# Performance work log

Measured on AMD Instinct MI355X. Metric: run time of the kernel, lower is better.

The kernel has to match this reference:

```python
import jax, jax.numpy as jnp
import numpy as np

B, R, C, A, K = 32, 13, 13, 5, 20
CELL = K + 5                      # 4 coords + objectness + 20 classes
N = R * C * A                     # 845 boxes per image
THRESH = 0.5
NMS_TH = 0.4
BIAS_VALS = [1.3221, 1.73145, 3.19275, 4.00944, 5.05587,
             8.09892, 9.47112, 4.84053, 11.2364, 10.0071]


def setup_inputs() -> dict:
    key = jax.random.key(0)
    x = jax.random.normal(key, (B, R, C, A * CELL), dtype=jnp.float32)
    bias = jnp.array(BIAS_VALS, dtype=jnp.float32)  # anchor priors (w,h interleaved)
    return {"x": x, "bias": bias}


def _nms_keep(iou, scores):
    """Greedy per-class NMS. iou: [B,N,N]; scores: [B,K,N] (already thresholded).
    Returns bool keep mask [B,K,N]. Decisions are non-differentiable, so inputs
    are stop_gradient'ed by the caller."""
    Bn = scores.shape[0]
    valid = scores > THRESH
    order = jnp.argsort(-scores, axis=-1)          # descending score order [B,K,N]
    rank = jnp.argsort(order, axis=-1)             # inverse permutation   [B,K,N]
    barange = jnp.arange(Bn)[:, None]

    def body(i, suppressed):
        idx = order[:, :, i]                                              # [B,K]
        sup_i = jnp.take_along_axis(suppressed, idx[:, :, None], -1)[..., 0]
        val_i = jnp.take_along_axis(valid, idx[:, :, None], -1)[..., 0]
        alive = val_i & ~sup_i                                            # [B,K]
        row = iou[barange, idx]                                           # [B,K,N]
        return suppressed | (alive[..., None] & (row > NMS_TH) & (rank > i))

    suppressed = jax.lax.fori_loop(0, N, body, jnp.zeros((Bn, K, N), bool))
    return valid & ~suppressed


def reference(x, bias):
    Bn, R_, C_, _ = x.shape
    t = x.reshape(Bn, R_, C_, A, CELL)
    gx = jnp.arange(C_, dtype=x.dtype)
    gy = jnp.arange(R_, dtype=x.dtype)
    # box decode (matches source: hNorm=rows used for width, wNorm=cols for height)
    bx = (jax.nn.sigmoid(t[..., 0]) + gx[None, None, :, None]) / C_
    by = (jax.nn.sigmoid(t[..., 1]) + gy[None, :, None, None]) / R_
    bw = jnp.exp(t[..., 2]) * bias[0::2] / R_
    bh = jnp.exp(t[..., 3]) * bias[1::2] / C_
    obj = jax.nn.sigmoid(t[..., 4])
    cls = jax.nn.softmax(t[..., 5:], axis=-1)
    prob = obj[..., None] * cls
    prob = jnp.where(prob > THRESH, prob, 0.0)

    # flatten to box index layout (y*cols + x)*anchors + a, same as source
    flat = lambda a: a.reshape(Bn, N)
    bx, by, bw, bh, obj = map(flat, (bx, by, bw, bh, obj))
    prob = prob.reshape(Bn, N, K)

    # corner-form boxes for IoU (source uses x - w/2, y - h/2, w, h)
    x1 = bx - bw * 0.5
    y1 = by - bh * 0.5
    x2 = x1 + bw
    y2 = y1 + bh
    iw = jnp.maximum(0.0, jnp.minimum(x2[:, :, None], x2[:, None, :]) -
                          jnp.maximum(x1[:, :, None], x1[:, None, :]))
    ih = jnp.maximum(0.0, jnp.minimum(y2[:, :, None], y2[:, None, :]) -
                          jnp.maximum(y1[:, :, None], y1[:, None, :]))
    inter = iw * ih
    area = bw * bh
    union = area[:, :, None] + area[:, None, :] - inter
    iou = inter / jnp.maximum(union, 1e-9)                       # [B,N,N]

    scores = prob.transpose(0, 2, 1)                             # [B,K,N]
    keep = _nms_keep(jax.lax.stop_gradient(iou),
                     jax.lax.stop_gradient(scores))
    out_prob = jnp.where(keep, scores, 0.0).transpose(0, 2, 1)   # [B,N,K]

    out = jnp.concatenate([bx[..., None], by[..., None], bw[..., None],
                           bh[..., None], obj[..., None], out_prob], axis=-1)
    return out  # [B, N, CELL]
```

## Files before the change

### kernel.cpp

```cpp
#include <hip/hip_runtime.h>
#include <math.h>

#define BN 32
#define RR 13
#define CC 13
#define AA 5
#define KK 20
#define CELLSZ 25
#define NN (RR * CC * AA)
#define NBK (BN * KK)
#define THRESH 0.5f
#define NMS_TH 0.4f

#define CAND_OFF 4096
#define REC 8
#define CAP NN

__device__ __forceinline__ float sigmoidf_(float x) {
    return 1.0f / (1.0f + expf(-x));
}

__global__ __launch_bounds__(256) void decode_kernel(
        const float* __restrict__ x,
        const float* __restrict__ bias,
        float* __restrict__ out,
        int* __restrict__ cnt,
        float* __restrict__ cand) {
    int idx = blockIdx.x * 256 + threadIdx.x;
    if (idx >= BN * NN) return;
    int b   = idx / NN;
    int n   = idx % NN;
    int r   = n / (CC * AA);
    int rem = n % (CC * AA);
    int c   = rem / AA;
    int a   = rem % AA;

    const float* t = x + (size_t)idx * CELLSZ;

    float bx  = (sigmoidf_(t[0]) + (float)c) / (float)CC;
    float by  = (sigmoidf_(t[1]) + (float)r) / (float)RR;
    float bw  = expf(t[2]) * bias[2 * a]     / (float)RR;
    float bh  = expf(t[3]) * bias[2 * a + 1] / (float)CC;
    float obj = sigmoidf_(t[4]);

    float l[KK];
    float m = t[5];
#pragma unroll
    for (int k = 0; k < KK; ++k) { l[k] = t[5 + k]; m = fmaxf(m, l[k]); }
    float s = 0.0f;
#pragma unroll
    for (int k = 0; k < KK; ++k) { l[k] = expf(l[k] - m); s += l[k]; }

    float* o = out + (size_t)idx * CELLSZ;
    o[0] = bx; o[1] = by; o[2] = bw; o[3] = bh; o[4] = obj;
#pragma unroll
    for (int k = 0; k < KK; ++k) o[5 + k] = 0.0f;

#pragma unroll
    for (int k = 0; k < KK; ++k) {
        float p = obj * (l[k] / s);
        if (p > THRESH) {
            int bk   = b * KK + k;
            int slot = atomicAdd(&cnt[bk], 1);
            float* rec = cand + ((size_t)bk * CAP + slot) * REC;
            float x1 = bx - bw * 0.5f;
            float y1 = by - bh * 0.5f;
            rec[0] = __int_as_float(n);
            rec[1] = p;
            rec[2] = x1;
            rec[3] = y1;
            rec[4] = x1 + bw;
            rec[5] = y1 + bh;
            rec[6] = bw * bh;
        }
    }
}

__global__ __launch_bounds__(64) void nms_kernel(
        const int* __restrict__ cnt,
        const float* __restrict__ cand,
        float* __restrict__ out) {
    int bk = blockIdx.x;
    int m  = cnt[bk];
    if (m <= 0) return;
    int b    = bk / KK;
    int k    = bk % KK;
    int lane = threadIdx.x;
    const float* list = cand + (size_t)bk * CAP * REC;

    if (m == 1) {
        if (lane == 0) {
            int n = __float_as_int(list[0]);
            out[((size_t)b * NN + n) * CELLSZ + 5 + k] = list[1];
        }
        return;
    }

    int T = (m + 63) >> 6;
    unsigned alive = 0;
    for (int tt = 0; tt < T; ++tt) {
        int j = lane + (tt << 6);
        if (j < m) alive |= 1u << tt;
    }

    while (true) {
        float bs = -1.0f;
        int   bn = 0x7fffffff;
        int   bg = -1;
        for (int tt = 0; tt < T; ++tt) {
            if ((alive >> tt) & 1u) {
                int j = lane + (tt << 6);
                float sc = list[j * REC + 1];
                int   nn = __float_as_int(list[j * REC]);
                if (sc > bs || (sc == bs && nn < bn)) { bs = sc; bn = nn; bg = j; }
            }
        }
#pragma unroll
        for (int off = 32; off > 0; off >>= 1) {
            float os = __shfl_xor(bs, off);
            int   on = __shfl_xor(bn, off);
            int   og = __shfl_xor(bg, off);
            if (os > bs || (os == bs && on < bn)) { bs = os; bn = on; bg = og; }
        }
        if (bg < 0) break;

        float X1 = list[bg * REC + 2];
        float Y1 = list[bg * REC + 3];
        float X2 = list[bg * REC + 4];
        float Y2 = list[bg * REC + 5];
        float AR = list[bg * REC + 6];

        if ((bg & 63) == lane) {
            out[((size_t)b * NN + bn) * CELLSZ + 5 + k] = bs;
            alive &= ~(1u << (bg >> 6));
        }

        for (int tt = 0; tt < T; ++tt) {
            int j = lane + (tt << 6);
            if (((alive >> tt) & 1u) && j != bg) {
                float iw = fmaxf(0.0f, fminf(X2, list[j * REC + 4]) - fmaxf(X1, list[j * REC + 2]));
                float ih = fmaxf(0.0f, fminf(Y2, list[j * REC + 5]) - fmaxf(Y1, list[j * REC + 3]));
                float inter = iw * ih;
                float uni   = AR + list[j * REC + 6] - inter;
                float iou   = inter / fmaxf(uni, 1e-9f);
                if (iou > NMS_TH) alive &= ~(1u << tt);
            }
        }
    }
}

extern "C" void kernel_launch(void* const* d_in, const int* in_sizes, int n_in,
                              void* d_out, int out_size, void* d_ws, size_t ws_size,
                              hipStream_t stream) {
    const float* x    = (const float*)d_in[0];
    const float* bias = (const float*)d_in[1];
    float* out = (float*)d_out;

    int*   cnt  = (int*)d_ws;
    float* cand = (float*)((char*)d_ws + CAND_OFF);

    hipMemsetAsync(cnt, 0, NBK * sizeof(int), stream);
    decode_kernel<<<(BN * NN + 255) / 256, 256, 0, stream>>>(x, bias, out, cnt, cand);
    nms_kernel<<<NBK, 64, 0, stream>>>(cnt, cand, out);
}
```

Baseline: 62.59 us.

## Fuse decode and per-class NMS into one block-per-image kernel using shared memory

Replaces the memset, decode kernel and per-(batch,class) NMS kernel with a single kernel that runs one 1024-thread block per image. The block stages the image in LDS, decodes there, and keeps candidate boxes in shared arrays; NMS then runs per class, one wave per class. It uses the fact that with threshold 0.5 only the argmax class can pass (two softmax probabilities cannot both exceed 0.5), so each box makes at most one candidate. This removes two launches, the global atomics and the global candidate round trip. In exchange only 32 blocks run, which leaves most CUs idle, and the shared-memory footprint is large.

```diff
diff --git a/kernel.cpp b/kernel.cpp
--- a/kernel.cpp
+++ b/kernel.cpp
@@ -8,145 +8,126 @@
 #define KK 20
 #define CELLSZ 25
 #define NN (RR * CC * AA)
-#define NBK (BN * KK)
+#define TOT (NN * CELLSZ)
 #define THRESH 0.5f
 #define NMS_TH 0.4f
+#define NT 1024
 
-#define CAND_OFF 4096
-#define REC 8
-#define CAP NN
-
-__device__ __forceinline__ float sigmoidf_(float x) {
-    return 1.0f / (1.0f + expf(-x));
-}
-
-__global__ __launch_bounds__(256) void decode_kernel(
+__global__ __launch_bounds__(NT) void region_kernel(
         const float* __restrict__ x,
         const float* __restrict__ bias,
-        float* __restrict__ out,
-        int* __restrict__ cnt,
-        float* __restrict__ cand) {
-    int idx = blockIdx.x * 256 + threadIdx.x;
-    if (idx >= BN * NN) return;
-    int b   = idx / NN;
-    int n   = idx % NN;
-    int r   = n / (CC * AA);
-    int rem = n % (CC * AA);
-    int c   = rem / AA;
-    int a   = rem % AA;
+        float* __restrict__ out)
+{
+    __shared__ float sraw[TOT];
+    __shared__ int   pcnt;
+    __shared__ int   kcnt[KK];
+    __shared__ int   ctag[NN], cidx[NN];
+    __shared__ float csc[NN], px1[NN], py1[NN], px2[NN], py2[NN], par[NN];
 
-    const float* t = x + (size_t)idx * CELLSZ;
+    const int b   = blockIdx.x;
+    const int tid = threadIdx.x;
+    const float* xb = x   + (size_t)b * TOT;
+    float*       ob = out + (size_t)b * TOT;
 
-    float bx  = (sigmoidf_(t[0]) + (float)c) / (float)CC;
-    float by  = (sigmoidf_(t[1]) + (float)r) / (float)RR;
-    float bw  = expf(t[2]) * bias[2 * a]     / (float)RR;
-    float bh  = expf(t[3]) * bias[2 * a + 1] / (float)CC;
-    float obj = sigmoidf_(t[4]);
+    if (tid == 0) pcnt = 0;
+    if (tid < KK) kcnt[tid] = 0;
 
-    float l[KK];
-    float m = t[5];
+    for (int i = tid; i < TOT; i += NT) sraw[i] = xb[i];
+    __syncthreads();
+
+    if (tid < NN) {
+        const int n  = tid;
+        int r   = n / (CC * AA);
+        int rem = n - r * (CC * AA);
+        int c   = rem / AA;
+        int a   = rem - c * AA;
+        float* t = sraw + n * CELLSZ;
+
+        float bx  = (1.f / (1.f + expf(-t[0])) + (float)c) / (float)CC;
+        float by  = (1.f / (1.f + expf(-t[1])) + (float)r) / (float)RR;
+        float bw  = expf(t[2]) * bias[2 * a]     / (float)RR;
+        float bh  = expf(t[3]) * bias[2 * a + 1] / (float)CC;
+        float obj = 1.f / (1.f + expf(-t[4]));
+
+        float l[KK];
+        float m = t[5];
 #pragma unroll
-    for (int k = 0; k < KK; ++k) { l[k] = t[5 + k]; m = fmaxf(m, l[k]); }
-    float s = 0.0f;
+        for (int k = 0; k < KK; ++k) { l[k] = t[5 + k]; m = fmaxf(m, l[k]); }
+        float s = 0.f;
 #pragma unroll
-    for (int k = 0; k < KK; ++k) { l[k] = expf(l[k] - m); s += l[k]; }
+        for (int k = 0; k < KK; ++k) s += expf(l[k] - m);
+        int km = 0;
+#pragma unroll
+        for (int k = 1; k < KK; ++k) if (l[k] > l[km]) km = k;
 
-    float* o = out + (size_t)idx * CELLSZ;
-    o[0] = bx; o[1] = by; o[2] = bw; o[3] = bh; o[4] = obj;
+        float p = obj * (1.0f / s);
+
+        t[0] = bx; t[1] = by; t[2] = bw; t[3] = bh; t[4] = obj;
 #pragma unroll
-    for (int k = 0; k < KK; ++k) o[5 + k] = 0.0f;
+        for (int k = 0; k < KK; ++k) t[5 + k] = 0.f;
 
-#pragma unroll
-    for (int k = 0; k < KK; ++k) {
-        float p = obj * (l[k] / s);
         if (p > THRESH) {
-            int bk   = b * KK + k;
-            int slot = atomicAdd(&cnt[bk], 1);
-            float* rec = cand + ((size_t)bk * CAP + slot) * REC;
-            float x1 = bx - bw * 0.5f;
-            float y1 = by - bh * 0.5f;
-            rec[0] = __int_as_float(n);
-            rec[1] = p;
-            rec[2] = x1;
-            rec[3] = y1;
-            rec[4] = x1 + bw;
-            rec[5] = y1 + bh;
-            rec[6] = bw * bh;
+            int slot = atomicAdd(&pcnt, 1);
+            atomicAdd(&kcnt[km], 1);
+            ctag[slot] = km; cidx[slot] = n; csc[slot] = p;
+            float x1 = bx - bw * 0.5f, y1 = by - bh * 0.5f;
+            px1[slot] = x1; py1[slot] = y1;
+            px2[slot] = x1 + bw; py2[slot] = y1 + bh;
+            par[slot] = bw * bh;
         }
     }
-}
+    __syncthreads();
 
-__global__ __launch_bounds__(64) void nms_kernel(
-        const int* __restrict__ cnt,
-        const float* __restrict__ cand,
-        float* __restrict__ out) {
-    int bk = blockIdx.x;
-    int m  = cnt[bk];
-    if (m <= 0) return;
-    int b    = bk / KK;
-    int k    = bk % KK;
-    int lane = threadIdx.x;
-    const float* list = cand + (size_t)bk * CAP * REC;
+    const int mtot = pcnt;
+    const int wave = tid >> 6;
+    const int lane = tid & 63;
+    const int T    = (mtot + 63) >> 6;
 
-    if (m == 1) {
-        if (lane == 0) {
-            int n = __float_as_int(list[0]);
-            out[((size_t)b * NN + n) * CELLSZ + 5 + k] = list[1];
-        }
-        return;
-    }
-
-    int T = (m + 63) >> 6;
-    unsigned alive = 0;
-    for (int tt = 0; tt < T; ++tt) {
-        int j = lane + (tt << 6);
-        if (j < m) alive |= 1u << tt;
-    }
-
-    while (true) {
-        float bs = -1.0f;
-        int   bn = 0x7fffffff;
-        int   bg = -1;
-        for (int tt = 0; tt < T; ++tt) {
-            if ((alive >> tt) & 1u) {
-                int j = lane + (tt << 6);
-                float sc = list[j * REC + 1];
-                int   nn = __float_as_int(list[j * REC]);
-                if (sc > bs || (sc == bs && nn < bn)) { bs = sc; bn = nn; bg = j; }
-            }
-        }
-#pragma unroll
-        for (int off = 32; off > 0; off >>= 1) {
-            float os = __shfl_xor(bs, off);
-            int   on = __shfl_xor(bn, off);
-            int   og = __shfl_xor(bg, off);
-            if (os > bs || (os == bs && on < bn)) { bs = os; bn = on; bg = og; }
-        }
-        if (bg < 0) break;
-
-        float X1 = list[bg * REC + 2];
-        float Y1 = list[bg * REC + 3];
-        float X2 = list[bg * REC + 4];
-        float Y2 = list[bg * REC + 5];
-        float AR = list[bg * REC + 6];
-
-        if ((bg & 63) == lane) {
-            out[((size_t)b * NN + bn) * CELLSZ + 5 + k] = bs;
-            alive &= ~(1u << (bg >> 6));
-        }
-
+    for (int k = wave; k < KK; k += (NT / 64)) {
+        if (kcnt[k] == 0) continue;
+        unsigned alive = 0;
         for (int tt = 0; tt < T; ++tt) {
             int j = lane + (tt << 6);
-            if (((alive >> tt) & 1u) && j != bg) {
-                float iw = fmaxf(0.0f, fminf(X2, list[j * REC + 4]) - fmaxf(X1, list[j * REC + 2]));
-                float ih = fmaxf(0.0f, fminf(Y2, list[j * REC + 5]) - fmaxf(Y1, list[j * REC + 3]));
-                float inter = iw * ih;
-                float uni   = AR + list[j * REC + 6] - inter;
-                float iou   = inter / fmaxf(uni, 1e-9f);
-                if (iou > NMS_TH) alive &= ~(1u << tt);
+            if (j < mtot && ctag[j] == k) alive |= (1u << tt);
+        }
+        while (true) {
+            float bs = -1.f; int bnn = 0x7fffffff; int bg = -1;
+            for (int tt = 0; tt < T; ++tt) {
+                if ((alive >> tt) & 1u) {
+                    int j = lane + (tt << 6);
+                    float sc = csc[j]; int nn = cidx[j];
+                    if (sc > bs || (sc == bs && nn < bnn)) { bs = sc; bnn = nn; bg = j; }
+                }
+            }
+#pragma unroll
+            for (int off = 32; off; off >>= 1) {
+                float os = __shfl_xor(bs, off);
+                int   on = __shfl_xor(bnn, off);
+                int   og = __shfl_xor(bg, off);
+                if (os > bs || (os == bs && on < bnn)) { bs = os; bnn = on; bg = og; }
+            }
+            if (bg < 0) break;
+
+            float X1 = px1[bg], Y1 = py1[bg], X2 = px2[bg], Y2 = py2[bg], AR = par[bg];
+            if ((bg & 63) == lane) {
+                sraw[bnn * CELLSZ + 5 + k] = bs;
+                alive &= ~(1u << (bg >> 6));
+            }
+            for (int tt = 0; tt < T; ++tt) {
+                int j = lane + (tt << 6);
+                if (((alive >> tt) & 1u) && j != bg) {
+                    float iw = fmaxf(0.f, fminf(X2, px2[j]) - fmaxf(X1, px1[j]));
+                    float ih = fmaxf(0.f, fminf(Y2, py2[j]) - fmaxf(Y1, py1[j]));
+                    float inter = iw * ih;
+                    float uni   = AR + par[j] - inter;
+                    if (inter / fmaxf(uni, 1e-9f) > NMS_TH) alive &= ~(1u << tt);
+                }
             }
         }
     }
+    __syncthreads();
+
+    for (int i = tid; i < TOT; i += NT) ob[i] = sraw[i];
 }
 
 extern "C" void kernel_launch(void* const* d_in, const int* in_sizes, int n_in,
@@ -156,10 +137,5 @@
     const float* bias = (const float*)d_in[1];
     float* out = (float*)d_out;
 
-    int*   cnt  = (int*)d_ws;
-    float* cand = (float*)((char*)d_ws + CAND_OFF);
-
-    hipMemsetAsync(cnt, 0, NBK * sizeof(int), stream);
-    decode_kernel<<<(BN * NN + 255) / 256, 256, 0, stream>>>(x, bias, out, cnt, cand);
-    nms_kernel<<<NBK, 64, 0, stream>>>(cnt, cand, out);
+    region_kernel<<<BN, NT, 0, stream>>>(x, bias, out);
 }
```

After: 65.32 us. +4.4%, slower.
